# Performance work log

Hardware: AMD Instinct MI355X
Metric: run time of the kernel (lower is better)

The kernel has to match this reference:

```python
import jax, jax.numpy as jnp
import numpy as np

N_NODE = 20000
N_EDGE = 200000
EMBED = 256
PAIR = 128
HEADS = 16
HEAD_DIM = EMBED // HEADS
SCALING = HEAD_DIM ** -0.5
EPS = 1e-5


def _ln(x, w, b):
    m = x.mean(-1, keepdims=True)
    v = ((x - m) ** 2).mean(-1, keepdims=True)
    return (x - m) / jnp.sqrt(v + EPS) * w + b


def setup_inputs() -> dict:
    key = jax.random.key(0)
    ks = jax.random.split(key, 12)
    inp = {
        "query": jax.random.normal(ks[0], (N_NODE, EMBED), jnp.float32),
        "edge_index": jax.random.randint(ks[1], (N_EDGE, 2), 0, N_NODE, jnp.int64 if jax.config.jax_enable_x64 else jnp.int32),
        "edge_diff": jax.random.normal(ks[2], (N_EDGE, 3), jnp.float32),
        "pair": jax.random.normal(ks[3], (N_EDGE, PAIR), jnp.float32),
        "ln_w": jnp.ones((EMBED,), jnp.float32),
        "ln_b": jnp.zeros((EMBED,), jnp.float32),
        "pln_w": jnp.ones((PAIR,), jnp.float32),
        "pln_b": jnp.zeros((PAIR,), jnp.float32),
        "Wq": jax.random.normal(ks[4], (EMBED, EMBED), jnp.float32) * 0.02,
        "Wk": jax.random.normal(ks[5], (EMBED, EMBED), jnp.float32) * 0.02,
        "Wv": jax.random.normal(ks[6], (EMBED, EMBED), jnp.float32) * 0.02,
        "Wb": jax.random.normal(ks[7], (HEADS, PAIR), jnp.float32) * 0.02,
        "bb": jnp.zeros((HEADS,), jnp.float32),
        "Wf1": jax.random.normal(ks[8], (1, EMBED), jnp.float32) * 0.02,
        "bf1": jnp.zeros((1,), jnp.float32),
        "Wf2": jax.random.normal(ks[9], (1, EMBED), jnp.float32) * 0.02,
        "bf2": jnp.zeros((1,), jnp.float32),
        "Wf3": jax.random.normal(ks[10], (1, EMBED), jnp.float32) * 0.02,
        "bf3": jnp.zeros((1,), jnp.float32),
    }
    return inp


def reference(query, edge_index, edge_diff, pair, ln_w, ln_b, pln_w, pln_b,
              Wq, Wk, Wv, Wb, bb, Wf1, bf1, Wf2, bf2, Wf3, bf3):
    n_node = query.shape[0]
    src = edge_index[:, 0]
    dst = edge_index[:, 1]

    qn = _ln(query, ln_w, ln_b)          # preln on node features
    pn = _ln(pair, pln_w, pln_b)         # preln on pair features

    q = (qn @ Wq.T).reshape(n_node, HEADS, HEAD_DIM)
    k = (qn @ Wk.T).reshape(n_node, HEADS, HEAD_DIM)
    v = (qn @ Wv.T).reshape(n_node, HEADS, HEAD_DIM)

    qe = q[src] * SCALING                # [E,H,D]
    ke = k[dst]
    ve = v[dst]

    logits = (qe * ke).sum(-1) + pn @ Wb.T + bb   # [E,H]

    # segment softmax over destination node (edge_index[:,0])
    seg_max = jax.ops.segment_max(logits, src, num_segments=n_node)  # [N,H]
    ex = jnp.exp(logits - seg_max[src])
    denom = jax.ops.segment_sum(ex, src, num_segments=n_node)
    probs = ex / denom[src]              # [E,H]

    # 3D-weighted scatter-sum: out[n,h,c,d] = sum_e probs[e,h]*diff[e,c]*v[e,h,d]
    w = probs[:, :, None] * edge_diff[:, None, :]                    # [E,H,3]
    contrib = w[:, :, :, None] * ve[:, :, None, :]                   # [E,H,3,D]
    x = jax.ops.segment_sum(contrib, src, num_segments=n_node)       # [N,H,3,D]
    x = x.transpose(0, 2, 1, 3).reshape(n_node, 3, EMBED)            # [N,3,H*D]

    f1 = x[:, 0, :] @ Wf1.T + bf1
    f2 = x[:, 1, :] @ Wf2.T + bf2
    f3 = x[:, 2, :] @ Wf3.T + bf3
    return jnp.concatenate([f1, f2, f3], axis=-1).astype(jnp.float32)
```

## Files before the change

### kernel.cpp

```cpp
#include <hip/hip_runtime.h>
#include <math.h>

#define N_NODE 20000
#define N_EDGE 200000
#define EMBED 256
#define PAIR 128
#define HEADS 16
#define HEAD_DIM 16
#define SCALING 0.25f
#define LNEPS 1e-5f

typedef unsigned short u16;
typedef unsigned int u32;
typedef __attribute__((ext_vector_type(8))) short bf16x8;
typedef __attribute__((ext_vector_type(4))) float f32x4;

#define WS_QKV   0
#define WS_QN    30720000
#define WS_WBF   40960000
#define WS_WW    41353216
#define WS_C0    41357312
#define WS_C1    41357376
#define WS_BIAS  41357440
#define WS_VW    54157440
#define WS_CNT   57997440
#define WS_CUR   58077440
#define WS_OFF   58157440
#define WS_DE    58237504

__device__ __forceinline__ u16 f2bf(float f) {
  u32 u = __float_as_uint(f);
  u32 r = (u + 0x7FFFu + ((u >> 16) & 1u)) >> 16;
  return (u16)r;
}
__device__ __forceinline__ float bl(u32 u) { return __uint_as_float(u << 16); }
__device__ __forceinline__ float bh(u32 u) { return __uint_as_float(u & 0xFFFF0000u); }

__device__ __forceinline__ float dot8(uint4 a, uint4 b) {
  float s = bl(a.x) * bl(b.x) + bh(a.x) * bh(b.x);
  s += bl(a.y) * bl(b.y) + bh(a.y) * bh(b.y);
  s += bl(a.z) * bl(b.z) + bh(a.z) * bh(b.z);
  s += bl(a.w) * bl(b.w) + bh(a.w) * bh(b.w);
  return s;
}

__global__ __launch_bounds__(256) void ln_qn_kernel(
    const float* __restrict__ query, const float* __restrict__ ln_w,
    const float* __restrict__ ln_b, u16* __restrict__ qn,
    int* __restrict__ counts, int* __restrict__ cur) {
  int z = blockIdx.x * 256 + threadIdx.x;
  if (z < N_NODE) { counts[z] = 0; cur[z] = 0; }
  int node = blockIdx.x * 4 + (threadIdx.x >> 6);
  int lane = threadIdx.x & 63;
  float4 a = *(const float4*)(query + (size_t)node * EMBED + lane * 4);
  float s = a.x + a.y + a.z + a.w;
  float s2 = a.x * a.x + a.y * a.y + a.z * a.z + a.w * a.w;
  #pragma unroll
  for (int off = 32; off > 0; off >>= 1) {
    s += __shfl_xor(s, off);
    s2 += __shfl_xor(s2, off);
  }
  float m = s * (1.0f / EMBED);
  float r = rsqrtf(s2 * (1.0f / EMBED) - m * m + LNEPS);
  float4 w4 = *(const float4*)(ln_w + lane * 4);
  float4 b4 = *(const float4*)(ln_b + lane * 4);
  ushort4 st;
  st.x = f2bf((a.x - m) * r * w4.x + b4.x);
  st.y = f2bf((a.y - m) * r * w4.y + b4.y);
  st.z = f2bf((a.z - m) * r * w4.z + b4.z);
  st.w = f2bf((a.w - m) * r * w4.w + b4.w);
  *(ushort4*)(qn + (size_t)node * EMBED + lane * 4) = st;
}

__global__ __launch_bounds__(256) void wcvt_prep_kernel(
    const float* __restrict__ Wq, const float* __restrict__ Wk,
    const float* __restrict__ Wv, u16* __restrict__ Wbf,
    const float* __restrict__ pln_w, const float* __restrict__ pln_b,
    const float* __restrict__ Wb, const float* __restrict__ bb,
    u16* __restrict__ WWbf, float* __restrict__ c0, float* __restrict__ c1) {
  if (blockIdx.x < 192) {
    int g4 = blockIdx.x * 256 + threadIdx.x;
    int idx = g4 * 4;
    const float* src = (idx < 65536) ? Wq : (idx < 131072 ? Wk : Wv);
    float4 v = *(const float4*)(src + (idx & 65535));
    ushort4 st = {f2bf(v.x), f2bf(v.y), f2bf(v.z), f2bf(v.w)};
    *(ushort4*)(Wbf + idx) = st;
  } else if (threadIdx.x < 64) {
    int l = threadIdx.x;
    for (int h = 0; h < HEADS; h++) {
      int i0 = l * 2;
      float wb0 = Wb[h * PAIR + i0], wb1 = Wb[h * PAIR + i0 + 1];
      float ww0 = pln_w[i0] * wb0, ww1 = pln_w[i0 + 1] * wb1;
      WWbf[h * PAIR + i0] = f2bf(ww0);
      WWbf[h * PAIR + i0 + 1] = f2bf(ww1);
      float s1 = ww0 + ww1;
      float s0 = pln_b[i0] * wb0 + pln_b[i0 + 1] * wb1;
      #pragma unroll
      for (int off = 32; off > 0; off >>= 1) {
        s1 += __shfl_xor(s1, off);
        s0 += __shfl_xor(s0, off);
      }
      if (l == 0) {
        c1[h] = s1;
        c0[h] = s0 + bb[h];
      }
    }
  }
}

#define GP 264
__global__ __launch_bounds__(256, 2) void qkv_gemm_kernel(
    const u16* __restrict__ qn, const u16* __restrict__ Wbf,
    u16* __restrict__ qkv) {
  __shared__ u16 As[64 * GP];
  __shared__ u16 Bs[64 * GP];
  int t = threadIdx.x;
  int wv = t >> 6, lane = t & 63;
  int quad = lane >> 4, l16 = lane & 15;
  int row0 = blockIdx.x * 64, col0 = blockIdx.y * 64;
  #pragma unroll
  for (int j = 0; j < 8; j++) {
    int row = j * 8 + (t >> 5);
    int slot = t & 31;
    int ra = min(row0 + row, N_NODE - 1);
    uint4 va = *(const uint4*)(qn + (size_t)ra * 256 + slot * 8);
    *(uint4*)(&As[row * GP + slot * 8]) = va;
    uint4 vb = *(const uint4*)(Wbf + (size_t)(col0 + row) * 256 + slot * 8);
    *(uint4*)(&Bs[row * GP + slot * 8]) = vb;
  }
  __syncthreads();
  int mt = (wv >> 1) * 32, nt = (wv & 1) * 32;
  f32x4 acc[2][2];
  #pragma unroll
  for (int im = 0; im < 2; im++)
    #pragma unroll
    for (int in_ = 0; in_ < 2; in_++) acc[im][in_] = (f32x4){0.f, 0.f, 0.f, 0.f};
  #pragma unroll
  for (int sk = 0; sk < 8; sk++) {
    int ko = sk * 32 + quad * 8;
    bf16x8 a0 = *(const bf16x8*)(&As[(mt + l16) * GP + ko]);
    bf16x8 a1 = *(const bf16x8*)(&As[(mt + 16 + l16) * GP + ko]);
    bf16x8 b0 = *(const bf16x8*)(&Bs[(nt + l16) * GP + ko]);
    bf16x8 b1 = *(const bf16x8*)(&Bs[(nt + 16 + l16) * GP + ko]);
    acc[0][0] = __builtin_amdgcn_mfma_f32_16x16x32_bf16(a0, b0, acc[0][0], 0, 0, 0);
    acc[0][1] = __builtin_amdgcn_mfma_f32_16x16x32_bf16(a0, b1, acc[0][1], 0, 0, 0);
    acc[1][0] = __builtin_amdgcn_mfma_f32_16x16x32_bf16(a1, b0, acc[1][0], 0, 0, 0);
    acc[1][1] = __builtin_amdgcn_mfma_f32_16x16x32_bf16(a1, b1, acc[1][1], 0, 0, 0);
  }
  float scale = (col0 < 256) ? SCALING : 1.0f;
  #pragma unroll
  for (int im = 0; im < 2; im++) {
    #pragma unroll
    for (int in_ = 0; in_ < 2; in_++) {
      #pragma unroll
      for (int r = 0; r < 4; r++) {
        int grow = row0 + mt + im * 16 + quad * 4 + r;
        int gcol = col0 + nt + in_ * 16 + l16;
        if (grow < N_NODE)
          qkv[(size_t)grow * 768 + gcol] = f2bf(acc[im][in_][r] * scale);
      }
    }
  }
}

__global__ __launch_bounds__(256) void vw_kernel(
    const u16* __restrict__ qkv, const float* __restrict__ Wf1,
    const float* __restrict__ Wf2, const float* __restrict__ Wf3,
    float* __restrict__ vw) {
  int gid = blockIdx.x * 256 + threadIdx.x;
  int n = gid >> 4, h = gid & 15;
  const uint4* vp = (const uint4*)(qkv + (size_t)n * 768 + 512 + h * 16);
  uint4 va = vp[0], vb = vp[1];
  float v[16];
  v[0] = bl(va.x); v[1] = bh(va.x); v[2] = bl(va.y); v[3] = bh(va.y);
  v[4] = bl(va.z); v[5] = bh(va.z); v[6] = bl(va.w); v[7] = bh(va.w);
  v[8] = bl(vb.x); v[9] = bh(vb.x); v[10] = bl(vb.y); v[11] = bh(vb.y);
  v[12] = bl(vb.z); v[13] = bh(vb.z); v[14] = bl(vb.w); v[15] = bh(vb.w);
  const float* wf[3] = {Wf1 + h * 16, Wf2 + h * 16, Wf3 + h * 16};
  #pragma unroll
  for (int c = 0; c < 3; c++) {
    float s = 0.f;
    #pragma unroll
    for (int d = 0; d < 16; d++) s += v[d] * wf[c][d];
    vw[(size_t)n * 48 + h * 3 + c] = s;
  }
}

#define PP 136
__global__ __launch_bounds__(256) void pair_bias_kernel(
    const float* __restrict__ pair, const u16* __restrict__ WWbf,
    const float* __restrict__ c0g, const float* __restrict__ c1g,
    float* __restrict__ bias) {
  __shared__ u16 Ps[64 * PP];
  __shared__ u16 WWs[16 * PP];
  __shared__ float ms[64], rs[64], c0s[16], c1s[16];
  int t = threadIdx.x;
  int wv = t >> 6, lane = t & 63;
  int quad = lane >> 4, l16 = lane & 15;
  int e0 = blockIdx.x * 64;
  #pragma unroll
  for (int j = 0; j < 8; j++) {
    int L = j * 256 + t;
    int row = L >> 5, slot = L & 31;
    float4 p = *(const float4*)(pair + (size_t)(e0 + row) * PAIR + slot * 4);
    ushort4 st = {f2bf(p.x), f2bf(p.y), f2bf(p.z), f2bf(p.w)};
    *(ushort4*)(&Ps[row * PP + slot * 4]) = st;
  }
  #pragma unroll
  for (int j = 0; j < 2; j++) {
    int L = j * 256 + t;
    int row = L >> 5, slot = L & 31;
    ushort4 w = *(const ushort4*)(WWbf + row * PAIR + slot * 4);
    *(ushort4*)(&WWs[row * PP + slot * 4]) = w;
  }
  if (t < 16) {
    c0s[t] = c0g[t];
    c1s[t] = c1g[t];
  }
  __syncthreads();
  {
    int row = t >> 2, qq = t & 3;
    float s = 0.f, s2 = 0.f;
    #pragma unroll
    for (int jj = 0; jj < 8; jj++) {
      ushort4 u = *(const ushort4*)(&Ps[row * PP + (qq * 8 + jj) * 4]);
      float x0 = __uint_as_float((u32)u.x << 16);
      float x1 = __uint_as_float((u32)u.y << 16);
      float x2 = __uint_as_float((u32)u.z << 16);
      float x3 = __uint_as_float((u32)u.w << 16);
      s += x0 + x1 + x2 + x3;
      s2 += x0 * x0 + x1 * x1 + x2 * x2 + x3 * x3;
    }
    s += __shfl_xor(s, 1); s += __shfl_xor(s, 2);
    s2 += __shfl_xor(s2, 1); s2 += __shfl_xor(s2, 2);
    if (qq == 0) {
      float m = s * (1.0f / PAIR);
      ms[row] = m;
      rs[row] = rsqrtf(s2 * (1.0f / PAIR) - m * m + LNEPS);
    }
  }
  __syncthreads();
  f32x4 acc = (f32x4){0.f, 0.f, 0.f, 0.f};
  #pragma unroll
  for (int sk = 0; sk < 4; sk++) {
    int ko = sk * 32 + quad * 8;
    bf16x8 a = *(const bf16x8*)(&Ps[(wv * 16 + l16) * PP + ko]);
    bf16x8 b = *(const bf16x8*)(&WWs[l16 * PP + ko]);
    acc = __builtin_amdgcn_mfma_f32_16x16x32_bf16(a, b, acc, 0, 0, 0);
  }
  #pragma unroll
  for (int r = 0; r < 4; r++) {
    int el = wv * 16 + quad * 4 + r;
    float bv = rs[el] * (acc[r] - ms[el] * c1s[l16]) + c0s[l16];
    bias[(size_t)(e0 + el) * HEADS + l16] = bv;
  }
}

__global__ __launch_bounds__(256) void hist_kernel(
    const int* __restrict__ edge_index, int* __restrict__ counts) {
  int e = blockIdx.x * 256 + threadIdx.x;
  if (e < N_EDGE) atomicAdd(&counts[edge_index[e * 2]], 1);
}

__global__ __launch_bounds__(1024) void scan_kernel(
    const int* __restrict__ counts, int* __restrict__ off) {
  __shared__ int part[1024];
  int t = threadIdx.x;
  int loc[20];
  int s = 0;
  #pragma unroll
  for (int i = 0; i < 20; i++) {
    int idx = t * 20 + i;
    int v = (idx < N_NODE) ? counts[idx] : 0;
    loc[i] = s;
    s += v;
  }
  part[t] = s;
  __syncthreads();
  int x = s;
  for (int o = 1; o < 1024; o <<= 1) {
    int y = (t >= o) ? part[t - o] : 0;
    __syncthreads();
    x += y;
    part[t] = x;
    __syncthreads();
  }
  int excl = x - s;
  #pragma unroll
  for (int i = 0; i < 20; i++) {
    int idx = t * 20 + i;
    if (idx < N_NODE) off[idx] = excl + loc[i];
  }
  if (t == 0) off[N_NODE] = N_EDGE;
}

__global__ __launch_bounds__(256) void scatter_kernel(
    const int* __restrict__ edge_index, const int* __restrict__ off,
    int* __restrict__ cur, int2* __restrict__ de) {
  int e = blockIdx.x * 256 + threadIdx.x;
  if (e >= N_EDGE) return;
  int src = edge_index[e * 2 + 0];
  int dst = edge_index[e * 2 + 1];
  int pos = off[src] + atomicAdd(&cur[src], 1);
  de[pos] = make_int2(dst, e);
}

__global__ __launch_bounds__(256) void seg_attn_kernel(
    const u16* __restrict__ qkv, const float* __restrict__ bias,
    const int* __restrict__ off, const int2* __restrict__ de,
    const float* __restrict__ vw, const float* __restrict__ edge_diff,
    const float* __restrict__ bf1, const float* __restrict__ bf2,
    const float* __restrict__ bf3, float* __restrict__ out) {
  int wv = threadIdx.x >> 6, lane = threadIdx.x & 63;
  int src = blockIdx.x * 4 + wv;
  int h = lane & 15, eslot = lane >> 4;
  int lo = off[src];
  int deg = off[src + 1] - lo;
  const uint4* qp = (const uint4*)(qkv + (size_t)src * 768 + h * 16);
  uint4 q0 = qp[0], q1 = qp[1];
  float exsum = 0.f, a0 = 0.f, a1 = 0.f, a2 = 0.f;
  for (int ei = eslot; ei < deg; ei += 4) {
    int2 d_e = de[lo + ei];
    const uint4* kp = (const uint4*)(qkv + (size_t)d_e.x * 768 + 256 + h * 16);
    float d = dot8(q0, kp[0]) + dot8(q1, kp[1]);
    float ex = __expf(d + bias[(size_t)d_e.y * HEADS + h]);
    exsum += ex;
    const float* vp = vw + (size_t)d_e.x * 48 + h * 3;
    const float* dp = edge_diff + (size_t)d_e.y * 3;
    a0 += ex * vp[0] * dp[0];
    a1 += ex * vp[1] * dp[1];
    a2 += ex * vp[2] * dp[2];
  }
  exsum += __shfl_xor(exsum, 16);
  exsum += __shfl_xor(exsum, 32);
  float rden = (exsum > 0.f) ? 1.0f / exsum : 0.f;
  a0 *= rden; a1 *= rden; a2 *= rden;
  #pragma unroll
  for (int o = 1; o < 64; o <<= 1) {
    a0 += __shfl_xor(a0, o);
    a1 += __shfl_xor(a1, o);
    a2 += __shfl_xor(a2, o);
  }
  if (lane == 0) {
    out[src * 3 + 0] = a0 + bf1[0];
    out[src * 3 + 1] = a1 + bf2[0];
    out[src * 3 + 2] = a2 + bf3[0];
  }
}

extern "C" void kernel_launch(void* const* d_in, const int* in_sizes, int n_in,
                              void* d_out, int out_size, void* d_ws,
                              size_t ws_size, hipStream_t stream) {
  const float* query      = (const float*)d_in[0];
  const int*   edge_index = (const int*)d_in[1];
  const float* edge_diff  = (const float*)d_in[2];
  const float* pair       = (const float*)d_in[3];
  const float* ln_w       = (const float*)d_in[4];
  const float* ln_b       = (const float*)d_in[5];
  const float* pln_w      = (const float*)d_in[6];
  const float* pln_b      = (const float*)d_in[7];
  const float* Wq         = (const float*)d_in[8];
  const float* Wk         = (const float*)d_in[9];
  const float* Wv         = (const float*)d_in[10];
  const float* Wb         = (const float*)d_in[11];
  const float* bb         = (const float*)d_in[12];
  const float* Wf1        = (const float*)d_in[13];
  const float* bf1        = (const float*)d_in[14];
  const float* Wf2        = (const float*)d_in[15];
  const float* bf2        = (const float*)d_in[16];
  const float* Wf3        = (const float*)d_in[17];
  const float* bf3        = (const float*)d_in[18];

  char* ws = (char*)d_ws;
  u16*   qkv   = (u16*)(ws + WS_QKV);
  u16*   qn    = (u16*)(ws + WS_QN);
  u16*   Wbf   = (u16*)(ws + WS_WBF);
  u16*   WWbf  = (u16*)(ws + WS_WW);
  float* c0    = (float*)(ws + WS_C0);
  float* c1    = (float*)(ws + WS_C1);
  float* bias  = (float*)(ws + WS_BIAS);
  float* vw    = (float*)(ws + WS_VW);
  int*   counts= (int*)(ws + WS_CNT);
  int*   cur   = (int*)(ws + WS_CUR);
  int*   off   = (int*)(ws + WS_OFF);
  int2*  de    = (int2*)(ws + WS_DE);
  float* out   = (float*)d_out;

  ln_qn_kernel<<<N_NODE / 4, 256, 0, stream>>>(query, ln_w, ln_b, qn, counts,
                                               cur);
  wcvt_prep_kernel<<<193, 256, 0, stream>>>(Wq, Wk, Wv, Wbf, pln_w, pln_b, Wb,
                                            bb, WWbf, c0, c1);
  dim3 ggrid((N_NODE + 63) / 64, 12);
  qkv_gemm_kernel<<<ggrid, 256, 0, stream>>>(qn, Wbf, qkv);
  vw_kernel<<<1250, 256, 0, stream>>>(qkv, Wf1, Wf2, Wf3, vw);
  pair_bias_kernel<<<N_EDGE / 64, 256, 0, stream>>>(pair, WWbf, c0, c1, bias);
  hist_kernel<<<(N_EDGE + 255) / 256, 256, 0, stream>>>(edge_index, counts);
  scan_kernel<<<1, 1024, 0, stream>>>(counts, off);
  scatter_kernel<<<(N_EDGE + 255) / 256, 256, 0, stream>>>(edge_index, off, cur,
                                                           de);
  seg_attn_kernel<<<N_NODE / 4, 256, 0, stream>>>(qkv, bias, off, de, vw,
                                                  edge_diff, bf1, bf2, bf3,
                                                  out);
}
```

Measured before the change: 314.0 us.

## Merge independent stages into three block-range-dispatched kernels to cut launches

Cuts the pipeline from nine launches to five by giving independent stages separate blockIdx ranges inside one kernel: LN plus weight conversion, QKV GEMM plus edge histogram, and pair bias plus vw projection plus CSR scatter. Each merged kernel picks its role from the block index. The aim is to remove launch gaps and tail idle time by letting small stages run alongside larger ones. In exchange, the merged kernels carry the GEMM's large shared-memory footprint and launch bounds into the cheap branches, which may lower occupancy for those blocks.

```diff
diff --git a/kernel.cpp b/kernel.cpp
--- a/kernel.cpp
+++ b/kernel.cpp
@@ -44,42 +44,41 @@
   return s;
 }
 
-__global__ __launch_bounds__(256) void ln_qn_kernel(
+__global__ __launch_bounds__(256) void k1_pre_kernel(
     const float* __restrict__ query, const float* __restrict__ ln_w,
     const float* __restrict__ ln_b, u16* __restrict__ qn,
-    int* __restrict__ counts, int* __restrict__ cur) {
-  int z = blockIdx.x * 256 + threadIdx.x;
-  if (z < N_NODE) { counts[z] = 0; cur[z] = 0; }
-  int node = blockIdx.x * 4 + (threadIdx.x >> 6);
-  int lane = threadIdx.x & 63;
-  float4 a = *(const float4*)(query + (size_t)node * EMBED + lane * 4);
-  float s = a.x + a.y + a.z + a.w;
-  float s2 = a.x * a.x + a.y * a.y + a.z * a.z + a.w * a.w;
-  #pragma unroll
-  for (int off = 32; off > 0; off >>= 1) {
-    s += __shfl_xor(s, off);
-    s2 += __shfl_xor(s2, off);
-  }
-  float m = s * (1.0f / EMBED);
-  float r = rsqrtf(s2 * (1.0f / EMBED) - m * m + LNEPS);
-  float4 w4 = *(const float4*)(ln_w + lane * 4);
-  float4 b4 = *(const float4*)(ln_b + lane * 4);
-  ushort4 st;
-  st.x = f2bf((a.x - m) * r * w4.x + b4.x);
-  st.y = f2bf((a.y - m) * r * w4.y + b4.y);
-  st.z = f2bf((a.z - m) * r * w4.z + b4.z);
-  st.w = f2bf((a.w - m) * r * w4.w + b4.w);
-  *(ushort4*)(qn + (size_t)node * EMBED + lane * 4) = st;
-}
-
-__global__ __launch_bounds__(256) void wcvt_prep_kernel(
+    int* __restrict__ counts, int* __restrict__ cur,
     const float* __restrict__ Wq, const float* __restrict__ Wk,
     const float* __restrict__ Wv, u16* __restrict__ Wbf,
     const float* __restrict__ pln_w, const float* __restrict__ pln_b,
     const float* __restrict__ Wb, const float* __restrict__ bb,
     u16* __restrict__ WWbf, float* __restrict__ c0, float* __restrict__ c1) {
-  if (blockIdx.x < 192) {
-    int g4 = blockIdx.x * 256 + threadIdx.x;
+  int bid = blockIdx.x;
+  if (bid < 5000) {
+    int z = bid * 256 + threadIdx.x;
+    if (z < N_NODE) { counts[z] = 0; cur[z] = 0; }
+    int node = bid * 4 + (threadIdx.x >> 6);
+    int lane = threadIdx.x & 63;
+    float4 a = *(const float4*)(query + (size_t)node * EMBED + lane * 4);
+    float s = a.x + a.y + a.z + a.w;
+    float s2 = a.x * a.x + a.y * a.y + a.z * a.z + a.w * a.w;
+    #pragma unroll
+    for (int off = 32; off > 0; off >>= 1) {
+      s += __shfl_xor(s, off);
+      s2 += __shfl_xor(s2, off);
+    }
+    float m = s * (1.0f / EMBED);
+    float r = rsqrtf(s2 * (1.0f / EMBED) - m * m + LNEPS);
+    float4 w4 = *(const float4*)(ln_w + lane * 4);
+    float4 b4 = *(const float4*)(ln_b + lane * 4);
+    ushort4 st;
+    st.x = f2bf((a.x - m) * r * w4.x + b4.x);
+    st.y = f2bf((a.y - m) * r * w4.y + b4.y);
+    st.z = f2bf((a.z - m) * r * w4.z + b4.z);
+    st.w = f2bf((a.w - m) * r * w4.w + b4.w);
+    *(ushort4*)(qn + (size_t)node * EMBED + lane * 4) = st;
+  } else if (bid < 5192) {
+    int g4 = (bid - 5000) * 256 + threadIdx.x;
     int idx = g4 * 4;
     const float* src = (idx < 65536) ? Wq : (idx < 131072 ? Wk : Wv);
     float4 v = *(const float4*)(src + (idx & 65535));
@@ -109,15 +108,23 @@
 }
 
 #define GP 264
-__global__ __launch_bounds__(256, 2) void qkv_gemm_kernel(
+__global__ __launch_bounds__(256, 2) void k2_gemm_hist_kernel(
     const u16* __restrict__ qn, const u16* __restrict__ Wbf,
-    u16* __restrict__ qkv) {
+    u16* __restrict__ qkv, const int* __restrict__ edge_index,
+    int* __restrict__ counts) {
   __shared__ u16 As[64 * GP];
   __shared__ u16 Bs[64 * GP];
+  int bid = blockIdx.x;
+  if (bid >= 3756) {
+    int e = (bid - 3756) * 256 + threadIdx.x;
+    if (e < N_EDGE) atomicAdd(&counts[edge_index[e * 2]], 1);
+    return;
+  }
+  int bx = bid % 313, by = bid / 313;
   int t = threadIdx.x;
   int wv = t >> 6, lane = t & 63;
   int quad = lane >> 4, l16 = lane & 15;
-  int row0 = blockIdx.x * 64, col0 = blockIdx.y * 64;
+  int row0 = bx * 64, col0 = by * 64;
   #pragma unroll
   for (int j = 0; j < 8; j++) {
     int row = j * 8 + (t >> 5);
@@ -163,41 +170,85 @@
   }
 }
 
-__global__ __launch_bounds__(256) void vw_kernel(
-    const u16* __restrict__ qkv, const float* __restrict__ Wf1,
-    const float* __restrict__ Wf2, const float* __restrict__ Wf3,
-    float* __restrict__ vw) {
-  int gid = blockIdx.x * 256 + threadIdx.x;
-  int n = gid >> 4, h = gid & 15;
-  const uint4* vp = (const uint4*)(qkv + (size_t)n * 768 + 512 + h * 16);
-  uint4 va = vp[0], vb = vp[1];
-  float v[16];
-  v[0] = bl(va.x); v[1] = bh(va.x); v[2] = bl(va.y); v[3] = bh(va.y);
-  v[4] = bl(va.z); v[5] = bh(va.z); v[6] = bl(va.w); v[7] = bh(va.w);
-  v[8] = bl(vb.x); v[9] = bh(vb.x); v[10] = bl(vb.y); v[11] = bh(vb.y);
-  v[12] = bl(vb.z); v[13] = bh(vb.z); v[14] = bl(vb.w); v[15] = bh(vb.w);
-  const float* wf[3] = {Wf1 + h * 16, Wf2 + h * 16, Wf3 + h * 16};
-  #pragma unroll
-  for (int c = 0; c < 3; c++) {
-    float s = 0.f;
-    #pragma unroll
-    for (int d = 0; d < 16; d++) s += v[d] * wf[c][d];
-    vw[(size_t)n * 48 + h * 3 + c] = s;
-  }
+__global__ __launch_bounds__(1024) void scan_kernel(
+    const int* __restrict__ counts, int* __restrict__ off) {
+  __shared__ int part[1024];
+  int t = threadIdx.x;
+  int loc[20];
+  int s = 0;
+  #pragma unroll
+  for (int i = 0; i < 20; i++) {
+    int idx = t * 20 + i;
+    int v = (idx < N_NODE) ? counts[idx] : 0;
+    loc[i] = s;
+    s += v;
+  }
+  part[t] = s;
+  __syncthreads();
+  int x = s;
+  for (int o = 1; o < 1024; o <<= 1) {
+    int y = (t >= o) ? part[t - o] : 0;
+    __syncthreads();
+    x += y;
+    part[t] = x;
+    __syncthreads();
+  }
+  int excl = x - s;
+  #pragma unroll
+  for (int i = 0; i < 20; i++) {
+    int idx = t * 20 + i;
+    if (idx < N_NODE) off[idx] = excl + loc[i];
+  }
+  if (t == 0) off[N_NODE] = N_EDGE;
 }
 
 #define PP 136
-__global__ __launch_bounds__(256) void pair_bias_kernel(
+__global__ __launch_bounds__(256) void k4_bias_vw_scatter_kernel(
     const float* __restrict__ pair, const u16* __restrict__ WWbf,
     const float* __restrict__ c0g, const float* __restrict__ c1g,
-    float* __restrict__ bias) {
+    float* __restrict__ bias, const u16* __restrict__ qkv,
+    const float* __restrict__ Wf1, const float* __restrict__ Wf2,
+    const float* __restrict__ Wf3, float* __restrict__ vw,
+    const int* __restrict__ edge_index, const int* __restrict__ off,
+    int* __restrict__ cur, int2* __restrict__ de) {
   __shared__ u16 Ps[64 * PP];
   __shared__ u16 WWs[16 * PP];
   __shared__ float ms[64], rs[64], c0s[16], c1s[16];
+  int bid = blockIdx.x;
   int t = threadIdx.x;
+  if (bid >= 4375) {
+    int e = (bid - 4375) * 256 + t;
+    if (e < N_EDGE) {
+      int src = edge_index[e * 2 + 0];
+      int dst = edge_index[e * 2 + 1];
+      int pos = off[src] + atomicAdd(&cur[src], 1);
+      de[pos] = make_int2(dst, e);
+    }
+    return;
+  }
+  if (bid >= 3125) {
+    int gid = (bid - 3125) * 256 + t;
+    int n = gid >> 4, h = gid & 15;
+    const uint4* vp = (const uint4*)(qkv + (size_t)n * 768 + 512 + h * 16);
+    uint4 va = vp[0], vb = vp[1];
+    float v[16];
+    v[0] = bl(va.x); v[1] = bh(va.x); v[2] = bl(va.y); v[3] = bh(va.y);
+    v[4] = bl(va.z); v[5] = bh(va.z); v[6] = bl(va.w); v[7] = bh(va.w);
+    v[8] = bl(vb.x); v[9] = bh(vb.x); v[10] = bl(vb.y); v[11] = bh(vb.y);
+    v[12] = bl(vb.z); v[13] = bh(vb.z); v[14] = bl(vb.w); v[15] = bh(vb.w);
+    const float* wf[3] = {Wf1 + h * 16, Wf2 + h * 16, Wf3 + h * 16};
+    #pragma unroll
+    for (int c = 0; c < 3; c++) {
+      float s = 0.f;
+      #pragma unroll
+      for (int d = 0; d < 16; d++) s += v[d] * wf[c][d];
+      vw[(size_t)n * 48 + h * 3 + c] = s;
+    }
+    return;
+  }
   int wv = t >> 6, lane = t & 63;
   int quad = lane >> 4, l16 = lane & 15;
-  int e0 = blockIdx.x * 64;
+  int e0 = bid * 64;
   #pragma unroll
   for (int j = 0; j < 8; j++) {
     int L = j * 256 + t;
@@ -254,55 +305,6 @@
     float bv = rs[el] * (acc[r] - ms[el] * c1s[l16]) + c0s[l16];
     bias[(size_t)(e0 + el) * HEADS + l16] = bv;
   }
-}
-
-__global__ __launch_bounds__(256) void hist_kernel(
-    const int* __restrict__ edge_index, int* __restrict__ counts) {
-  int e = blockIdx.x * 256 + threadIdx.x;
-  if (e < N_EDGE) atomicAdd(&counts[edge_index[e * 2]], 1);
-}
-
-__global__ __launch_bounds__(1024) void scan_kernel(
-    const int* __restrict__ counts, int* __restrict__ off) {
-  __shared__ int part[1024];
-  int t = threadIdx.x;
-  int loc[20];
-  int s = 0;
-  #pragma unroll
-  for (int i = 0; i < 20; i++) {
-    int idx = t * 20 + i;
-    int v = (idx < N_NODE) ? counts[idx] : 0;
-    loc[i] = s;
-    s += v;
-  }
-  part[t] = s;
-  __syncthreads();
-  int x = s;
-  for (int o = 1; o < 1024; o <<= 1) {
-    int y = (t >= o) ? part[t - o] : 0;
-    __syncthreads();
-    x += y;
-    part[t] = x;
-    __syncthreads();
-  }
-  int excl = x - s;
-  #pragma unroll
-  for (int i = 0; i < 20; i++) {
-    int idx = t * 20 + i;
-    if (idx < N_NODE) off[idx] = excl + loc[i];
-  }
-  if (t == 0) off[N_NODE] = N_EDGE;
-}
-
-__global__ __launch_bounds__(256) void scatter_kernel(
-    const int* __restrict__ edge_index, const int* __restrict__ off,
-    int* __restrict__ cur, int2* __restrict__ de) {
-  int e = blockIdx.x * 256 + threadIdx.x;
-  if (e >= N_EDGE) return;
-  int src = edge_index[e * 2 + 0];
-  int dst = edge_index[e * 2 + 1];
-  int pos = off[src] + atomicAdd(&cur[src], 1);
-  de[pos] = make_int2(dst, e);
 }
 
 __global__ __launch_bounds__(256) void seg_attn_kernel(
@@ -386,18 +388,15 @@
   int2*  de    = (int2*)(ws + WS_DE);
   float* out   = (float*)d_out;
 
-  ln_qn_kernel<<<N_NODE / 4, 256, 0, stream>>>(query, ln_w, ln_b, qn, counts,
-                                               cur);
-  wcvt_prep_kernel<<<193, 256, 0, stream>>>(Wq, Wk, Wv, Wbf, pln_w, pln_b, Wb,
-                                            bb, WWbf, c0, c1);
-  dim3 ggrid((N_NODE + 63) / 64, 12);
-  qkv_gemm_kernel<<<ggrid, 256, 0, stream>>>(qn, Wbf, qkv);
-  vw_kernel<<<1250, 256, 0, stream>>>(qkv, Wf1, Wf2, Wf3, vw);
-  pair_bias_kernel<<<N_EDGE / 64, 256, 0, stream>>>(pair, WWbf, c0, c1, bias);
-  hist_kernel<<<(N_EDGE + 255) / 256, 256, 0, stream>>>(edge_index, counts);
+  k1_pre_kernel<<<5193, 256, 0, stream>>>(query, ln_w, ln_b, qn, counts, cur,
+                                          Wq, Wk, Wv, Wbf, pln_w, pln_b, Wb,
+                                          bb, WWbf, c0, c1);
+  k2_gemm_hist_kernel<<<4538, 256, 0, stream>>>(qn, Wbf, qkv, edge_index,
+                                                counts);
   scan_kernel<<<1, 1024, 0, stream>>>(counts, off);
-  scatter_kernel<<<(N_EDGE + 255) / 256, 256, 0, stream>>>(edge_index, off, cur,
-                                                           de);
+  k4_bias_vw_scatter_kernel<<<5157, 256, 0, stream>>>(
+      pair, WWbf, c0, c1, bias, qkv, Wf1, Wf2, Wf3, vw, edge_index, off, cur,
+      de);
   seg_attn_kernel<<<N_NODE / 4, 256, 0, stream>>>(qkv, bias, off, de, vw,
                                                   edge_diff, bf1, bf2, bf3,
                                                   out);
```

Measured after the change: 295.8 us. 1.06x faster.
